# Optimization experiments

Hardware: AMD Instinct MI355X
Metric: run time of the kernel (lower is better)

The kernel has to match this reference:

```python
import jax, jax.numpy as jnp
import numpy as np

L, S, N, E, H = 2048, 2048, 4, 1024, 16
D = E // H  # head_dim = 64


def setup_inputs() -> dict:
    key = jax.random.key(0)
    ks = jax.random.split(key, 7)
    scale = 1.0 / np.sqrt(E)
    return {
        "query": jax.random.normal(ks[0], (L, N, E), jnp.float32),
        "key": jax.random.normal(ks[1], (S, N, E), jnp.float32),
        "value": jax.random.normal(ks[2], (S, N, E), jnp.float32),
        "in_proj_w": jax.random.normal(ks[3], (3 * E, E), jnp.float32) * scale,
        "in_proj_b": jax.random.normal(ks[4], (3 * E,), jnp.float32) * 0.01,
        "out_proj_w": jax.random.normal(ks[5], (E, E), jnp.float32) * scale * 0.25,
        "out_proj_b": jax.random.normal(ks[6], (E,), jnp.float32) * 0.01,
    }


def reference(query, key, value, in_proj_w, in_proj_b, out_proj_w, out_proj_b):
    # Split packed in-projection into q/k/v parts (torch layout: [3E, E]).
    wq, wk, wv = in_proj_w[:E], in_proj_w[E:2 * E], in_proj_w[2 * E:]
    bq, bk, bv = in_proj_b[:E], in_proj_b[E:2 * E], in_proj_b[2 * E:]

    def proj(x, w, b):  # (T,N,E) -> (N,H,T,D)
        y = jnp.einsum('tne,fe->tnf', x, w) + b
        T = x.shape[0]
        return y.reshape(T, N, H, D).transpose(1, 2, 0, 3)

    q = proj(query, wq, bq) * (1.0 / np.sqrt(D))  # scale queries
    k = proj(key, wk, bk)
    v = proj(value, wv, bv)

    scores = jnp.einsum('nhld,nhsd->nhls', q, k)  # (N,H,L,S)
    attn = jax.nn.softmax(scores, axis=-1)
    ctx = jnp.einsum('nhls,nhsd->nhld', attn, v)  # (N,H,L,D)
    ctx = ctx.transpose(2, 0, 1, 3).reshape(L, N, E)  # (L,N,E)

    out = jnp.einsum('lne,fe->lnf', ctx, out_proj_w) + out_proj_b
    attn_weights = attn.mean(axis=1)  # (N,L,S), averaged over heads (torch default)
    return out, attn_weights
```

## Files before the change

### kernel.cpp

```cpp
#include <hip/hip_runtime.h>
#include <hip/hip_bf16.h>

#define L_ 2048
#define S_ 2048
#define NB 4
#define E_ 1024
#define H_ 16
#define D_ 64
#define LDT 72
#define NCH (S_ / 64)

typedef __attribute__((ext_vector_type(8))) short bf16x8;
typedef __attribute__((ext_vector_type(4))) float f32x4;

__device__ __forceinline__ short f2bf(float f) {
  union { float f; unsigned u; } v; v.f = f;
  unsigned r = v.u + 0x7FFFu + ((v.u >> 16) & 1u);
  return (short)(r >> 16);
}
__device__ __forceinline__ float bf2f(short s) {
  union { unsigned u; float f; } v; v.u = ((unsigned)(unsigned short)s) << 16;
  return v.f;
}
__device__ __forceinline__ unsigned cvt_pk_bf16(float lo, float hi) {
  unsigned r;
  asm("v_cvt_pk_bf16_f32 %0, %1, %2" : "=v"(r) : "v"(lo), "v"(hi));
  return r;
}

#define LGKM_BARRIER() do {                                   \
    asm volatile("s_waitcnt lgkmcnt(0)" ::: "memory");        \
    __builtin_amdgcn_sched_barrier(0);                        \
    __builtin_amdgcn_s_barrier();                             \
    __builtin_amdgcn_sched_barrier(0);                        \
  } while (0)

__global__ void k_convert(const float* __restrict__ wi, const float* __restrict__ wo,
                          short* __restrict__ wqkv, short* __restrict__ wout) {
  const int n1 = 3 * E_ * E_ / 4;
  const int n2 = E_ * E_ / 4;
  const int stride = gridDim.x * blockDim.x;
  for (int i = blockIdx.x * blockDim.x + threadIdx.x; i < n1 + n2; i += stride) {
    const float4* s; short* d; int j;
    if (i < n1) { s = (const float4*)wi; d = wqkv; j = i; }
    else        { s = (const float4*)wo; d = wout; j = i - n1; }
    float4 v = s[j];
    uint2 o; o.x = cvt_pk_bf16(v.x, v.y); o.y = cvt_pk_bf16(v.z, v.w);
    *(uint2*)&d[(size_t)j * 4] = o;
  }
}

__global__ __launch_bounds__(256) void k_qkv(
    const float* __restrict__ qin, const float* __restrict__ kin, const float* __restrict__ vin,
    const short* __restrict__ wbf, const float* __restrict__ bias,
    short* __restrict__ qh, short* __restrict__ kh, short* __restrict__ vt) {
  __shared__ short As[128 * LDT];
  __shared__ short Bs[128 * LDT];
  const int bm = blockIdx.x;
  const int fbase = blockIdx.y * 128;
  const int mat = fbase >> 10;
  const float* __restrict__ A = (mat == 0) ? qin : (mat == 1) ? kin : vin;
  short* __restrict__ dst = (mat == 0) ? qh : (mat == 1) ? kh : vt;
  const float scale = (mat == 0) ? 0.125f * 1.44269504088896f : 1.0f;
  const int tid = threadIdx.x;
  const int lane = tid & 63, wid = tid >> 6;
  const int wr = wid >> 1, wc = wid & 1;
  const int lr = lane & 15, lk = lane >> 4;
  f32x4 acc[4][4] = {};

  for (int kb = 0; kb < E_; kb += 64) {
#pragma unroll
    for (int i = 0; i < 8; ++i) {
      int f4 = i * 256 + tid;
      int row = f4 >> 4, k4 = f4 & 15;
      float4 v = *(const float4*)&A[(size_t)(bm * 128 + row) * E_ + kb + k4 * 4];
      uint2 o; o.x = cvt_pk_bf16(v.x, v.y); o.y = cvt_pk_bf16(v.z, v.w);
      *(uint2*)&As[row * LDT + k4 * 4] = o;
    }
#pragma unroll
    for (int i = 0; i < 4; ++i) {
      int e8 = i * 256 + tid;
      int row = e8 >> 3, k8 = e8 & 7;
      int4 v = *(const int4*)&wbf[(size_t)(fbase + row) * E_ + kb + k8 * 8];
      *(int4*)&Bs[row * LDT + k8 * 8] = v;
    }
    __syncthreads();
#pragma unroll
    for (int kk = 0; kk < 2; ++kk) {
      bf16x8 a[4], b[4];
#pragma unroll
      for (int fi = 0; fi < 4; ++fi)
        a[fi] = *(const bf16x8*)&As[(wr * 64 + fi * 16 + lr) * LDT + kk * 32 + lk * 8];
#pragma unroll
      for (int ci = 0; ci < 4; ++ci)
        b[ci] = *(const bf16x8*)&Bs[(wc * 64 + ci * 16 + lr) * LDT + kk * 32 + lk * 8];
#pragma unroll
      for (int fi = 0; fi < 4; ++fi)
#pragma unroll
        for (int ci = 0; ci < 4; ++ci)
          acc[fi][ci] = __builtin_amdgcn_mfma_f32_16x16x32_bf16(a[fi], b[ci], acc[fi][ci], 0, 0, 0);
    }
    __syncthreads();
  }
#pragma unroll
  for (int ci = 0; ci < 4; ++ci) {
    const int fg = fbase + wc * 64 + ci * 16 + lr;
    const float b = bias[fg];
    const int col = fg & 1023;
    const int h = col >> 6, d = col & 63;
#pragma unroll
    for (int fi = 0; fi < 4; ++fi)
#pragma unroll
      for (int j = 0; j < 4; ++j) {
        int m = bm * 128 + wr * 64 + fi * 16 + lk * 4 + j;
        int t = m >> 2, n = m & 3;
        float vv = (acc[fi][ci][j] + b) * scale;
        size_t base = (size_t)(n * H_ + h) * (L_ * D_);
        size_t idx = (mat == 2)
          ? base + (size_t)(t >> 5) * (D_ * 32) + d * 32 + (t & 31)
          : base + ((size_t)t << 6) + d;
        dst[idx] = f2bf(vv);
      }
  }
}

__global__ __launch_bounds__(256) void k_stats(
    const short* __restrict__ qh, const short* __restrict__ kh, float* __restrict__ rl) {
  const int nh = blockIdx.y;
  const int qt = blockIdx.x;
  const short* __restrict__ Q = qh + (size_t)nh * L_ * D_;
  const short* __restrict__ K = kh + (size_t)nh * S_ * D_;
  const int tid = threadIdx.x;
  const int lane = tid & 63, wid = tid >> 6;
  const int lr = lane & 15, lk = lane >> 4;
  const int rbase = qt * 128 + wid * 32;
  bf16x8 a[2][2];
#pragma unroll
  for (int ri = 0; ri < 2; ++ri)
#pragma unroll
    for (int kk = 0; kk < 2; ++kk)
      a[ri][kk] = *(const bf16x8*)&Q[(size_t)(rbase + ri * 16 + lr) * D_ + kk * 32 + lk * 8];
  bf16x8 kst[4][2];
#pragma unroll
  for (int ci = 0; ci < 4; ++ci) {
    kst[ci][0] = *(const bf16x8*)&K[(size_t)(ci * 16 + lr) * D_ + lk * 8];
    kst[ci][1] = *(const bf16x8*)&K[(size_t)(ci * 16 + lr) * D_ + 32 + lk * 8];
  }
  float ssum[2][4] = {};
  for (int st = 0; st < S_; st += 64) {
    const int stn = (st + 64 < S_) ? st + 64 : st;
    f32x4 acc[2][4] = {};
#pragma unroll
    for (int ci = 0; ci < 4; ++ci) {
#pragma unroll
      for (int ri = 0; ri < 2; ++ri) {
        acc[ri][ci] = __builtin_amdgcn_mfma_f32_16x16x32_bf16(a[ri][0], kst[ci][0], acc[ri][ci], 0, 0, 0);
        acc[ri][ci] = __builtin_amdgcn_mfma_f32_16x16x32_bf16(a[ri][1], kst[ci][1], acc[ri][ci], 0, 0, 0);
      }
      kst[ci][0] = *(const bf16x8*)&K[(size_t)(stn + ci * 16 + lr) * D_ + lk * 8];
      kst[ci][1] = *(const bf16x8*)&K[(size_t)(stn + ci * 16 + lr) * D_ + 32 + lk * 8];
    }
#pragma unroll
    for (int ri = 0; ri < 2; ++ri)
#pragma unroll
      for (int j = 0; j < 4; ++j) {
        float s = __builtin_amdgcn_exp2f(acc[ri][0][j]) + __builtin_amdgcn_exp2f(acc[ri][1][j]) +
                  __builtin_amdgcn_exp2f(acc[ri][2][j]) + __builtin_amdgcn_exp2f(acc[ri][3][j]);
        s += __shfl_xor(s, 1);
        s += __shfl_xor(s, 2);
        s += __shfl_xor(s, 4);
        s += __shfl_xor(s, 8);
        ssum[ri][j] += s;
      }
  }
  if (lr == 0) {
#pragma unroll
    for (int ri = 0; ri < 2; ++ri)
#pragma unroll
      for (int j = 0; j < 4; ++j)
        rl[(size_t)nh * L_ + rbase + ri * 16 + lk * 4 + j] = 1.0f / ssum[ri][j];
  }
}

__global__ __launch_bounds__(1024) void k_attn(
    const short* __restrict__ qh, const short* __restrict__ kh, const short* __restrict__ vt,
    const float* __restrict__ rl, float* __restrict__ attnw, short* __restrict__ ctx) {
  extern __shared__ char psl[];
  const int bid = blockIdx.x;
  const int xcd = bid & 7;
  const int n = xcd >> 1;
  const int qt = (bid >> 3) | ((xcd & 1) << 5);
  const int tid = threadIdx.x;
  const int h = tid >> 6, lane = tid & 63;
  const int lr = lane & 15, lk = lane >> 4;
  const int rbase = qt * 32;
  const size_t nh = (size_t)(n * H_ + h);
  const short* __restrict__ K = kh + nh * S_ * D_;
  const short* __restrict__ VT = vt + nh * S_ * D_;
  char* const slab0 = psl + h * 4096;

  bf16x8 qf[2][2];
  float rls[2];
  {
    const short* Q = qh + nh * L_ * D_;
#pragma unroll
    for (int li = 0; li < 2; ++li) {
#pragma unroll
      for (int kk = 0; kk < 2; ++kk)
        qf[li][kk] = *(const bf16x8*)&Q[(size_t)(rbase + li * 16 + lr) * D_ + kk * 32 + lk * 8];
      rls[li] = rl[nh * L_ + rbase + li * 16 + lr];
    }
  }
  f32x4 cacc[2][4] = {};
  const int mrow = tid >> 4, mc4 = (tid & 15) * 4;
  float* awp = attnw + ((size_t)n * L_ + rbase + mrow) * S_ + mc4;
  const int moff = mrow * 128 + ((mc4 * 2) ^ ((mrow & 7) << 4));

  for (int ch = 0; ch < NCH; ++ch) {
    const int st = ch * 64;
    char* const sl = slab0 + (ch & 1) * 65536;
    bf16x8 kf[4][2];
#pragma unroll
    for (int u = 0; u < 4; ++u) {
      kf[u][0] = *(const bf16x8*)&K[(size_t)(st + u * 16 + lr) * D_ + lk * 8];
      kf[u][1] = *(const bf16x8*)&K[(size_t)(st + u * 16 + lr) * D_ + 32 + lk * 8];
    }
    bf16x8 vb[4][2];
#pragma unroll
    for (int b = 0; b < 2; ++b) {
      const size_t sb = (size_t)((st >> 5) + b) * (D_ * 32);
#pragma unroll
      for (int ci = 0; ci < 4; ++ci)
        vb[ci][b] = *(const bf16x8*)&VT[sb + (ci * 16 + lr) * 32 + lk * 8];
    }
#pragma unroll
    for (int u = 0; u < 4; ++u) {
#pragma unroll
      for (int li = 0; li < 2; ++li) {
        f32x4 sc = {};
        __builtin_amdgcn_s_setprio(1);
        sc = __builtin_amdgcn_mfma_f32_16x16x32_bf16(kf[u][0], qf[li][0], sc, 0, 0, 0);
        sc = __builtin_amdgcn_mfma_f32_16x16x32_bf16(kf[u][1], qf[li][1], sc, 0, 0, 0);
        __builtin_amdgcn_s_setprio(0);
        uint2 pk;
        pk.x = cvt_pk_bf16(__builtin_amdgcn_exp2f(sc[0]) * rls[li],
                           __builtin_amdgcn_exp2f(sc[1]) * rls[li]);
        pk.y = cvt_pk_bf16(__builtin_amdgcn_exp2f(sc[2]) * rls[li],
                           __builtin_amdgcn_exp2f(sc[3]) * rls[li]);
        const int row = li * 16 + lr;
        *(uint2*)(sl + row * 128 + ((u * 32 + lk * 8) ^ ((row & 7) << 4))) = pk;
      }
    }
#pragma unroll
    for (int b = 0; b < 2; ++b)
#pragma unroll
      for (int li = 0; li < 2; ++li) {
        const int row = li * 16 + lr;
        bf16x8 pa = *(const bf16x8*)(sl + row * 128 + ((b * 64 + lk * 16) ^ ((row & 7) << 4)));
        __builtin_amdgcn_s_setprio(1);
#pragma unroll
        for (int ci = 0; ci < 4; ++ci)
          cacc[li][ci] = __builtin_amdgcn_mfma_f32_16x16x32_bf16(pa, vb[ci][b], cacc[li][ci], 0, 0, 0);
        __builtin_amdgcn_s_setprio(0);
      }
    if (ch > 0 && tid < 512) {
      char* const ms = psl + (((ch & 1) ^ 1)) * 65536;
      float s0 = 0.f, s1 = 0.f, s2 = 0.f, s3 = 0.f;
#pragma unroll
      for (int hh = 0; hh < 16; ++hh) {
        uint2 m = *(const uint2*)(ms + hh * 4096 + moff);
        s0 += bf2f((short)(m.x & 0xFFFF)); s1 += bf2f((short)(m.x >> 16));
        s2 += bf2f((short)(m.y & 0xFFFF)); s3 += bf2f((short)(m.y >> 16));
      }
      *(float4*)&awp[st - 64] = make_float4(s0 * 0.0625f, s1 * 0.0625f,
                                            s2 * 0.0625f, s3 * 0.0625f);
    }
    LGKM_BARRIER();
  }
  if (tid < 512) {
    char* const ms = psl + 65536;
    float s0 = 0.f, s1 = 0.f, s2 = 0.f, s3 = 0.f;
#pragma unroll
    for (int hh = 0; hh < 16; ++hh) {
      uint2 m = *(const uint2*)(ms + hh * 4096 + moff);
      s0 += bf2f((short)(m.x & 0xFFFF)); s1 += bf2f((short)(m.x >> 16));
      s2 += bf2f((short)(m.y & 0xFFFF)); s3 += bf2f((short)(m.y >> 16));
    }
    *(float4*)&awp[S_ - 64] = make_float4(s0 * 0.0625f, s1 * 0.0625f,
                                          s2 * 0.0625f, s3 * 0.0625f);
  }
#pragma unroll
  for (int li = 0; li < 2; ++li)
#pragma unroll
    for (int ci = 0; ci < 4; ++ci)
#pragma unroll
      for (int j = 0; j < 4; ++j) {
        int row = rbase + li * 16 + lk * 4 + j;
        int d = ci * 16 + lr;
        ctx[((size_t)row * NB + n) * E_ + h * 64 + d] = f2bf(cacc[li][ci][j]);
      }
}

__global__ __launch_bounds__(256) void k_out(
    const short* __restrict__ ctxb, const short* __restrict__ wbf,
    const float* __restrict__ bias, float* __restrict__ out) {
  __shared__ short As[128 * LDT];
  __shared__ short Bs[128 * LDT];
  const int bm = blockIdx.x, bn = blockIdx.y;
  const int tid = threadIdx.x;
  const int lane = tid & 63, wid = tid >> 6;
  const int wr = wid >> 1, wc = wid & 1;
  const int lr = lane & 15, lk = lane >> 4;
  f32x4 acc[4][4] = {};
  for (int kb = 0; kb < E_; kb += 64) {
#pragma unroll
    for (int i = 0; i < 4; ++i) {
      int e8 = i * 256 + tid;
      int row = e8 >> 3, k8 = e8 & 7;
      int4 va = *(const int4*)&ctxb[(size_t)(bm * 128 + row) * E_ + kb + k8 * 8];
      *(int4*)&As[row * LDT + k8 * 8] = va;
      int4 vb = *(const int4*)&wbf[(size_t)(bn * 128 + row) * E_ + kb + k8 * 8];
      *(int4*)&Bs[row * LDT + k8 * 8] = vb;
    }
    __syncthreads();
#pragma unroll
    for (int kk = 0; kk < 2; ++kk) {
      bf16x8 a[4], b[4];
#pragma unroll
      for (int fi = 0; fi < 4; ++fi)
        a[fi] = *(const bf16x8*)&As[(wr * 64 + fi * 16 + lr) * LDT + kk * 32 + lk * 8];
#pragma unroll
      for (int ci = 0; ci < 4; ++ci)
        b[ci] = *(const bf16x8*)&Bs[(wc * 64 + ci * 16 + lr) * LDT + kk * 32 + lk * 8];
#pragma unroll
      for (int fi = 0; fi < 4; ++fi)
#pragma unroll
        for (int ci = 0; ci < 4; ++ci)
          acc[fi][ci] = __builtin_amdgcn_mfma_f32_16x16x32_bf16(a[fi], b[ci], acc[fi][ci], 0, 0, 0);
    }
    __syncthreads();
  }
#pragma unroll
  for (int ci = 0; ci < 4; ++ci) {
    int col = bn * 128 + wc * 64 + ci * 16 + lr;
    float b = bias[col];
#pragma unroll
    for (int fi = 0; fi < 4; ++fi)
#pragma unroll
      for (int j = 0; j < 4; ++j) {
        int m = bm * 128 + wr * 64 + fi * 16 + lk * 4 + j;
        out[(size_t)m * E_ + col] = acc[fi][ci][j] + b;
      }
  }
}

extern "C" void kernel_launch(void* const* d_in, const int* in_sizes, int n_in,
                              void* d_out, int out_size, void* d_ws, size_t ws_size,
                              hipStream_t stream) {
  const float* qin = (const float*)d_in[0];
  const float* kin = (const float*)d_in[1];
  const float* vin = (const float*)d_in[2];
  const float* wi  = (const float*)d_in[3];
  const float* bi  = (const float*)d_in[4];
  const float* wo  = (const float*)d_in[5];
  const float* bo  = (const float*)d_in[6];
  float* out = (float*)d_out;
  float* attnw = out + (size_t)L_ * NB * E_;

  short* wqkv = (short*)d_ws;
  short* wout = wqkv + (size_t)3 * E_ * E_;
  short* qh = wout + (size_t)E_ * E_;
  short* kh = qh + (size_t)NB * L_ * E_;
  short* vt = kh + (size_t)NB * L_ * E_;
  float* rl = (float*)(vt + (size_t)NB * L_ * E_);
  short* ctx = (short*)(rl + (size_t)NB * H_ * L_);

  k_convert<<<1024, 256, 0, stream>>>(wi, wo, wqkv, wout);
  k_qkv<<<dim3(64, 24), 256, 0, stream>>>(qin, kin, vin, wqkv, bi, qh, kh, vt);
  k_stats<<<dim3(16, 64), 256, 0, stream>>>(qh, kh, rl);
  k_attn<<<256, 1024, 131072, stream>>>(qh, kh, vt, rl, attnw, ctx);
  k_out<<<dim3(64, 8), 256, 0, stream>>>(ctx, wout, bo, out);
}
```

Before: 495.5 us.

## Pre-convert activations to bf16 and stage GEMM tiles via direct global-to-LDS loads

Activations are now converted to bf16 in the conversion kernel, so the QKV GEMM reads bf16 and, like the output GEMM, fills shared memory with global_load_lds 16-byte transfers instead of register round-trips. The padded LDS stride is dropped to fit that load pattern, which may add bank conflicts on MFMA operand reads. The attention kernel also spreads the head-average of attention weights over all 1024 threads in 2-wide chunks instead of 512 threads in 4-wide chunks, and removes the setprio hints around the MFMAs. The extra bf16 activation buffers cost an additional pass over the inputs, and ctx reuses the xq buffer.

```diff
diff --git a/kernel.cpp b/kernel.cpp
--- a/kernel.cpp
+++ b/kernel.cpp
@@ -7,7 +7,6 @@
 #define E_ 1024
 #define H_ 16
 #define D_ 64
-#define LDT 72
 #define NCH (S_ / 64)
 
 typedef __attribute__((ext_vector_type(8))) short bf16x8;
@@ -26,6 +25,11 @@
   unsigned r;
   asm("v_cvt_pk_bf16_f32 %0, %1, %2" : "=v"(r) : "v"(lo), "v"(hi));
   return r;
+}
+__device__ __forceinline__ void gld16(const void* g, void* l) {
+  __builtin_amdgcn_global_load_lds(
+      (const __attribute__((address_space(1))) unsigned*)g,
+      (__attribute__((address_space(3))) unsigned*)l, 16, 0, 0);
 }
 
 #define LGKM_BARRIER() do {                                   \
@@ -36,53 +40,63 @@
   } while (0)
 
 __global__ void k_convert(const float* __restrict__ wi, const float* __restrict__ wo,
-                          short* __restrict__ wqkv, short* __restrict__ wout) {
+                          const float* __restrict__ qin, const float* __restrict__ kin,
+                          const float* __restrict__ vin,
+                          short* __restrict__ wqkv, short* __restrict__ wout,
+                          short* __restrict__ xq, short* __restrict__ xk,
+                          short* __restrict__ xv) {
   const int n1 = 3 * E_ * E_ / 4;
   const int n2 = E_ * E_ / 4;
+  const int n3 = L_ * NB * E_ / 4;
+  const int total = n1 + n2 + 3 * n3;
   const int stride = gridDim.x * blockDim.x;
-  for (int i = blockIdx.x * blockDim.x + threadIdx.x; i < n1 + n2; i += stride) {
-    const float4* s; short* d; int j;
-    if (i < n1) { s = (const float4*)wi; d = wqkv; j = i; }
-    else        { s = (const float4*)wo; d = wout; j = i - n1; }
-    float4 v = s[j];
+  for (int i = blockIdx.x * blockDim.x + threadIdx.x; i < total; i += stride) {
+    const float* src; short* dst; int j = i;
+    if (j < n1) { src = wi; dst = wqkv; }
+    else {
+      j -= n1;
+      if (j < n2) { src = wo; dst = wout; }
+      else {
+        j -= n2;
+        if (j < n3) { src = qin; dst = xq; }
+        else {
+          j -= n3;
+          if (j < n3) { src = kin; dst = xk; }
+          else { j -= n3; src = vin; dst = xv; }
+        }
+      }
+    }
+    float4 v = ((const float4*)src)[j];
     uint2 o; o.x = cvt_pk_bf16(v.x, v.y); o.y = cvt_pk_bf16(v.z, v.w);
-    *(uint2*)&d[(size_t)j * 4] = o;
+    *(uint2*)&dst[(size_t)j * 4] = o;
   }
 }
 
 __global__ __launch_bounds__(256) void k_qkv(
-    const float* __restrict__ qin, const float* __restrict__ kin, const float* __restrict__ vin,
+    const short* __restrict__ xq, const short* __restrict__ xk, const short* __restrict__ xv,
     const short* __restrict__ wbf, const float* __restrict__ bias,
     short* __restrict__ qh, short* __restrict__ kh, short* __restrict__ vt) {
-  __shared__ short As[128 * LDT];
-  __shared__ short Bs[128 * LDT];
+  __shared__ short As[128 * 64];
+  __shared__ short Bs[128 * 64];
   const int bm = blockIdx.x;
   const int fbase = blockIdx.y * 128;
   const int mat = fbase >> 10;
-  const float* __restrict__ A = (mat == 0) ? qin : (mat == 1) ? kin : vin;
+  const short* __restrict__ A = (mat == 0) ? xq : (mat == 1) ? xk : xv;
   short* __restrict__ dst = (mat == 0) ? qh : (mat == 1) ? kh : vt;
   const float scale = (mat == 0) ? 0.125f * 1.44269504088896f : 1.0f;
   const int tid = threadIdx.x;
   const int lane = tid & 63, wid = tid >> 6;
   const int wr = wid >> 1, wc = wid & 1;
   const int lr = lane & 15, lk = lane >> 4;
+  const int srow = lane >> 3, schk = (lane & 7) * 8;
   f32x4 acc[4][4] = {};
 
   for (int kb = 0; kb < E_; kb += 64) {
 #pragma unroll
-    for (int i = 0; i < 8; ++i) {
-      int f4 = i * 256 + tid;
-      int row = f4 >> 4, k4 = f4 & 15;
-      float4 v = *(const float4*)&A[(size_t)(bm * 128 + row) * E_ + kb + k4 * 4];
-      uint2 o; o.x = cvt_pk_bf16(v.x, v.y); o.y = cvt_pk_bf16(v.z, v.w);
-      *(uint2*)&As[row * LDT + k4 * 4] = o;
-    }
-#pragma unroll
     for (int i = 0; i < 4; ++i) {
-      int e8 = i * 256 + tid;
-      int row = e8 >> 3, k8 = e8 & 7;
-      int4 v = *(const int4*)&wbf[(size_t)(fbase + row) * E_ + kb + k8 * 8];
-      *(int4*)&Bs[row * LDT + k8 * 8] = v;
+      const int row0 = wid * 32 + i * 8;
+      gld16(&A[(size_t)(bm * 128 + row0 + srow) * E_ + kb + schk], &As[row0 * 64]);
+      gld16(&wbf[(size_t)(fbase + row0 + srow) * E_ + kb + schk], &Bs[row0 * 64]);
     }
     __syncthreads();
 #pragma unroll
@@ -90,10 +104,10 @@
       bf16x8 a[4], b[4];
 #pragma unroll
       for (int fi = 0; fi < 4; ++fi)
-        a[fi] = *(const bf16x8*)&As[(wr * 64 + fi * 16 + lr) * LDT + kk * 32 + lk * 8];
+        a[fi] = *(const bf16x8*)&As[(wr * 64 + fi * 16 + lr) * 64 + kk * 32 + lk * 8];
 #pragma unroll
       for (int ci = 0; ci < 4; ++ci)
-        b[ci] = *(const bf16x8*)&Bs[(wc * 64 + ci * 16 + lr) * LDT + kk * 32 + lk * 8];
+        b[ci] = *(const bf16x8*)&Bs[(wc * 64 + ci * 16 + lr) * 64 + kk * 32 + lk * 8];
 #pragma unroll
       for (int fi = 0; fi < 4; ++fi)
 #pragma unroll
@@ -212,9 +226,9 @@
     }
   }
   f32x4 cacc[2][4] = {};
-  const int mrow = tid >> 4, mc4 = (tid & 15) * 4;
-  float* awp = attnw + ((size_t)n * L_ + rbase + mrow) * S_ + mc4;
-  const int moff = mrow * 128 + ((mc4 * 2) ^ ((mrow & 7) << 4));
+  const int mrow = tid >> 5, mc2 = (tid & 31) * 2;
+  float* awp = attnw + ((size_t)n * L_ + rbase + mrow) * S_ + mc2;
+  const int moff = mrow * 128 + ((mc2 * 2) ^ ((mrow & 7) << 4));
 
   for (int ch = 0; ch < NCH; ++ch) {
     const int st = ch * 64;
@@ -238,10 +252,8 @@
 #pragma unroll
       for (int li = 0; li < 2; ++li) {
         f32x4 sc = {};
-        __builtin_amdgcn_s_setprio(1);
         sc = __builtin_amdgcn_mfma_f32_16x16x32_bf16(kf[u][0], qf[li][0], sc, 0, 0, 0);
         sc = __builtin_amdgcn_mfma_f32_16x16x32_bf16(kf[u][1], qf[li][1], sc, 0, 0, 0);
-        __builtin_amdgcn_s_setprio(0);
         uint2 pk;
         pk.x = cvt_pk_bf16(__builtin_amdgcn_exp2f(sc[0]) * rls[li],
                            __builtin_amdgcn_exp2f(sc[1]) * rls[li]);
@@ -257,37 +269,31 @@
       for (int li = 0; li < 2; ++li) {
         const int row = li * 16 + lr;
         bf16x8 pa = *(const bf16x8*)(sl + row * 128 + ((b * 64 + lk * 16) ^ ((row & 7) << 4)));
-        __builtin_amdgcn_s_setprio(1);
 #pragma unroll
         for (int ci = 0; ci < 4; ++ci)
           cacc[li][ci] = __builtin_amdgcn_mfma_f32_16x16x32_bf16(pa, vb[ci][b], cacc[li][ci], 0, 0, 0);
-        __builtin_amdgcn_s_setprio(0);
-      }
-    if (ch > 0 && tid < 512) {
+      }
+    if (ch > 0) {
       char* const ms = psl + (((ch & 1) ^ 1)) * 65536;
-      float s0 = 0.f, s1 = 0.f, s2 = 0.f, s3 = 0.f;
+      float s0 = 0.f, s1 = 0.f;
 #pragma unroll
       for (int hh = 0; hh < 16; ++hh) {
-        uint2 m = *(const uint2*)(ms + hh * 4096 + moff);
-        s0 += bf2f((short)(m.x & 0xFFFF)); s1 += bf2f((short)(m.x >> 16));
-        s2 += bf2f((short)(m.y & 0xFFFF)); s3 += bf2f((short)(m.y >> 16));
-      }
-      *(float4*)&awp[st - 64] = make_float4(s0 * 0.0625f, s1 * 0.0625f,
-                                            s2 * 0.0625f, s3 * 0.0625f);
+        short2 m = *(const short2*)(ms + hh * 4096 + moff);
+        s0 += bf2f(m.x); s1 += bf2f(m.y);
+      }
+      *(float2*)&awp[st - 64] = make_float2(s0 * 0.0625f, s1 * 0.0625f);
     }
     LGKM_BARRIER();
   }
-  if (tid < 512) {
+  {
     char* const ms = psl + 65536;
-    float s0 = 0.f, s1 = 0.f, s2 = 0.f, s3 = 0.f;
+    float s0 = 0.f, s1 = 0.f;
 #pragma unroll
     for (int hh = 0; hh < 16; ++hh) {
-      uint2 m = *(const uint2*)(ms + hh * 4096 + moff);
-      s0 += bf2f((short)(m.x & 0xFFFF)); s1 += bf2f((short)(m.x >> 16));
-      s2 += bf2f((short)(m.y & 0xFFFF)); s3 += bf2f((short)(m.y >> 16));
-    }
-    *(float4*)&awp[S_ - 64] = make_float4(s0 * 0.0625f, s1 * 0.0625f,
-                                          s2 * 0.0625f, s3 * 0.0625f);
+      short2 m = *(const short2*)(ms + hh * 4096 + moff);
+      s0 += bf2f(m.x); s1 += bf2f(m.y);
+    }
+    *(float2*)&awp[S_ - 64] = make_float2(s0 * 0.0625f, s1 * 0.0625f);
   }
 #pragma unroll
   for (int li = 0; li < 2; ++li)
@@ -304,23 +310,21 @@
 __global__ __launch_bounds__(256) void k_out(
     const short* __restrict__ ctxb, const short* __restrict__ wbf,
     const float* __restrict__ bias, float* __restrict__ out) {
-  __shared__ short As[128 * LDT];
-  __shared__ short Bs[128 * LDT];
+  __shared__ short As[128 * 64];
+  __shared__ short Bs[128 * 64];
   const int bm = blockIdx.x, bn = blockIdx.y;
   const int tid = threadIdx.x;
   const int lane = tid & 63, wid = tid >> 6;
   const int wr = wid >> 1, wc = wid & 1;
   const int lr = lane & 15, lk = lane >> 4;
+  const int srow = lane >> 3, schk = (lane & 7) * 8;
   f32x4 acc[4][4] = {};
   for (int kb = 0; kb < E_; kb += 64) {
 #pragma unroll
     for (int i = 0; i < 4; ++i) {
-      int e8 = i * 256 + tid;
-      int row = e8 >> 3, k8 = e8 & 7;
-      int4 va = *(const int4*)&ctxb[(size_t)(bm * 128 + row) * E_ + kb + k8 * 8];
-      *(int4*)&As[row * LDT + k8 * 8] = va;
-      int4 vb = *(const int4*)&wbf[(size_t)(bn * 128 + row) * E_ + kb + k8 * 8];
-      *(int4*)&Bs[row * LDT + k8 * 8] = vb;
+      const int row0 = wid * 32 + i * 8;
+      gld16(&ctxb[(size_t)(bm * 128 + row0 + srow) * E_ + kb + schk], &As[row0 * 64]);
+      gld16(&wbf[(size_t)(bn * 128 + row0 + srow) * E_ + kb + schk], &Bs[row0 * 64]);
     }
     __syncthreads();
 #pragma unroll
@@ -328,10 +332,10 @@
       bf16x8 a[4], b[4];
 #pragma unroll
       for (int fi = 0; fi < 4; ++fi)
-        a[fi] = *(const bf16x8*)&As[(wr * 64 + fi * 16 + lr) * LDT + kk * 32 + lk * 8];
+        a[fi] = *(const bf16x8*)&As[(wr * 64 + fi * 16 + lr) * 64 + kk * 32 + lk * 8];
 #pragma unroll
       for (int ci = 0; ci < 4; ++ci)
-        b[ci] = *(const bf16x8*)&Bs[(wc * 64 + ci * 16 + lr) * LDT + kk * 32 + lk * 8];
+        b[ci] = *(const bf16x8*)&Bs[(wc * 64 + ci * 16 + lr) * 64 + kk * 32 + lk * 8];
 #pragma unroll
       for (int fi = 0; fi < 4; ++fi)
 #pragma unroll
@@ -373,10 +377,13 @@
   short* kh = qh + (size_t)NB * L_ * E_;
   short* vt = kh + (size_t)NB * L_ * E_;
   float* rl = (float*)(vt + (size_t)NB * L_ * E_);
-  short* ctx = (short*)(rl + (size_t)NB * H_ * L_);
-
-  k_convert<<<1024, 256, 0, stream>>>(wi, wo, wqkv, wout);
-  k_qkv<<<dim3(64, 24), 256, 0, stream>>>(qin, kin, vin, wqkv, bi, qh, kh, vt);
+  short* xq = (short*)(rl + (size_t)NB * H_ * L_);
+  short* xk = xq + (size_t)L_ * NB * E_;
+  short* xv = xk + (size_t)L_ * NB * E_;
+  short* ctx = xq;
+
+  k_convert<<<2048, 256, 0, stream>>>(wi, wo, qin, kin, vin, wqkv, wout, xq, xk, xv);
+  k_qkv<<<dim3(64, 24), 256, 0, stream>>>(xq, xk, xv, wqkv, bi, qh, kh, vt);
   k_stats<<<dim3(16, 64), 256, 0, stream>>>(qh, kh, rl);
   k_attn<<<256, 1024, 131072, stream>>>(qh, kh, vt, rl, attnw, ctx);
   k_out<<<dim3(64, 8), 256, 0, stream>>>(ctx, wout, bo, out);
```

New measurement: 463.5 us. 6.4% less time.
